# Kernel optimization log

Hardware: AMD Instinct MI355X
Metric: run time of the kernel (lower is better)

The kernel has to match this reference:

```python
import jax, jax.numpy as jnp
import numpy as np


def setup_inputs() -> dict:
    key = jax.random.key(0)
    k0, k1, k2, k3, k4, k5 = jax.random.split(key, 6)
    L1, L2, B, D = 512, 512, 32, 1024
    inputs1 = jax.random.normal(k0, (L1, B, D), dtype=jnp.float32)
    inputs2 = jax.random.normal(k1, (L2, B, D), dtype=jnp.float32)
    # mask value 0 marks a valid token (module keeps pairs where both masks == 0)
    mask1 = jax.random.randint(k2, (L1, B), 0, 2, dtype=jnp.int64)
    mask2 = jax.random.randint(k3, (L2, B), 0, 2, dtype=jnp.int64)
    W = jax.random.normal(k4, (D, D), dtype=jnp.float32) * 0.02
    b = jax.random.normal(k5, (1,), dtype=jnp.float32) * 0.02
    return {"inputs1": inputs1, "inputs2": inputs2, "mask1": mask1,
            "mask2": mask2, "W": W, "b": b, "k": 256}


def reference(inputs1, inputs2, mask1, mask2, W, b, k):
    # inputs: [len, bsz, hdim]; masks: [len, bsz]
    H1 = jnp.transpose(inputs1, (1, 0, 2))  # [B, L1, D]
    H2 = jnp.transpose(inputs2, (1, 0, 2))  # [B, L2, D]
    # bilinear scores: H1 @ W @ H2^T + b, then relu  -> [B, L1, L2]
    S = jax.nn.relu(jnp.einsum('bid,de,bje->bij', H1, W, H2) + b[0])
    # pair is valid iff both mask entries are 0
    valid = (mask1.T[:, :, None] == 0) & (mask2.T[:, None, :] == 0)  # [B, L1, L2]
    B = S.shape[0]
    S_flat = jnp.where(valid.reshape(B, -1), S.reshape(B, -1), -jnp.inf)
    num_elems = S_flat.shape[1]
    k_actual = min(k, num_elems)
    q, _ = jax.lax.top_k(S_flat, k_actual)  # [B, k_actual]
    # replace -inf tail entries with the last finite value in each row
    neg = jnp.isneginf(q)
    q_num_finite = k_actual - neg.sum(axis=-1)  # [B]
    fill = jnp.take_along_axis(q, (q_num_finite - 1)[:, None], axis=1)  # [B, 1]
    q = jnp.where(neg, fill, q)
    if k_actual < k:
        q = jnp.concatenate(
            [q, jnp.broadcast_to(q[:, -1:], (B, k - k_actual))], axis=1)
    return q
```

## Files before the change

kernel.cpp:

```cpp
#include <hip/hip_runtime.h>

typedef __bf16 bf16_t;
typedef bf16_t bf16x8 __attribute__((ext_vector_type(8)));
typedef float floatx4 __attribute__((ext_vector_type(4)));

#define L1C 512
#define L2C 512
#define BC  32
#define DC  1024
#define KTOP 256
#define NBIN 4096
#define CAP  1024
#define FBUF 16384

__device__ __forceinline__ unsigned short f2bf(float f) {
    unsigned u = __float_as_uint(f);
    u += 0x7FFFu + ((u >> 16) & 1u);
    return (unsigned short)(u >> 16);
}

__device__ __forceinline__ void g2l16(const unsigned short* g, unsigned short* l) {
    __builtin_amdgcn_global_load_lds((const unsigned int*)g, (unsigned int*)l,
                                     16, 0, 0);
}

__device__ __forceinline__ float decode_key(unsigned k) {
    return __uint_as_float(k & 0x7FFFFFFFu);
}

__global__ __launch_bounds__(256) void prep_kernel(
    const float* __restrict__ in1, const float* __restrict__ in2,
    const float* __restrict__ W,
    const int* __restrict__ mask1, const int* __restrict__ mask2,
    unsigned short* __restrict__ A1, unsigned short* __restrict__ A2,
    unsigned short* __restrict__ Wb,
    int* __restrict__ m1t, int* __restrict__ m2t,
    unsigned* __restrict__ cnt) {
    int r = blockIdx.x, t = threadIdx.x;
    if (r < 2 * L1C * BC + DC) {
        const float* src;
        unsigned short* dst;
        if (r < L1C * BC) {
            int l = r >> 5, b = r & 31;
            src = in1 + (size_t)r * DC;
            dst = A1 + ((size_t)b * L1C + l) * DC;
        } else if (r < 2 * L1C * BC) {
            int r2 = r - L1C * BC;
            int l = r2 >> 5, b = r2 & 31;
            src = in2 + (size_t)r2 * DC;
            dst = A2 + ((size_t)b * L2C + l) * DC;
        } else {
            int r3 = r - 2 * L1C * BC;
            src = W + (size_t)r3 * DC;
            dst = Wb + (size_t)r3 * DC;
        }
        float4 v = reinterpret_cast<const float4*>(src)[t];
        ushort4 o;
        o.x = f2bf(v.x); o.y = f2bf(v.y); o.z = f2bf(v.z); o.w = f2bf(v.w);
        reinterpret_cast<ushort4*>(dst)[t] = o;
    } else {
        int gid = (r - (2 * L1C * BC + DC)) * 256 + t;
        int l = gid & 511, b = gid >> 9;
        m1t[gid] = mask1[(l << 5) + b];
        m2t[gid] = mask2[(l << 5) + b];
        if (gid < BC * 16) cnt[gid] = 0;
    }
}

__global__ __launch_bounds__(256) void gemm1_kernel(
    const unsigned short* __restrict__ A,
    const unsigned short* __restrict__ Bt,
    unsigned short* __restrict__ C) {
    __shared__ unsigned short As[128][64];
    __shared__ unsigned short Bs[128][64];
    int tid = threadIdx.x;
    int wave = tid >> 6, lane = tid & 63;
    int lane15 = lane & 15, quad = lane >> 4;
    int wm = wave >> 1, wn = wave & 1;
    size_t m0 = (size_t)blockIdx.x * 128, n0 = (size_t)blockIdx.y * 128;

    floatx4 zero = {0.f, 0.f, 0.f, 0.f};
    floatx4 acc[4][4];
#pragma unroll
    for (int i = 0; i < 4; i++)
#pragma unroll
        for (int j = 0; j < 4; j++) acc[i][j] = zero;

    for (int k0 = 0; k0 < DC; k0 += 64) {
#pragma unroll
        for (int c = 0; c < 4; c++) {
            int cid = c * 256 + tid;
            int row = cid >> 3, col8 = (cid & 7) * 8;
            unsigned short* lbase = &As[0][0] + (c * 256 + wave * 64) * 8;
            g2l16(&A[(m0 + row) * DC + k0 + col8], lbase);
            unsigned short* lbase2 = &Bs[0][0] + (c * 256 + wave * 64) * 8;
            g2l16(&Bt[(n0 + row) * DC + k0 + col8], lbase2);
        }
        __syncthreads();
#pragma unroll
        for (int kk = 0; kk < 64; kk += 32) {
            bf16x8 af[4], bfr[4];
#pragma unroll
            for (int mi = 0; mi < 4; mi++)
                af[mi] = *reinterpret_cast<const bf16x8*>(
                    &As[wm * 64 + mi * 16 + lane15][kk + quad * 8]);
#pragma unroll
            for (int ni = 0; ni < 4; ni++)
                bfr[ni] = *reinterpret_cast<const bf16x8*>(
                    &Bs[wn * 64 + ni * 16 + lane15][kk + quad * 8]);
#pragma unroll
            for (int mi = 0; mi < 4; mi++)
#pragma unroll
                for (int ni = 0; ni < 4; ni++)
                    acc[mi][ni] = __builtin_amdgcn_mfma_f32_16x16x32_bf16(
                        af[mi], bfr[ni], acc[mi][ni], 0, 0, 0);
        }
        __syncthreads();
    }
#pragma unroll
    for (int mi = 0; mi < 4; mi++)
#pragma unroll
        for (int ni = 0; ni < 4; ni++)
#pragma unroll
            for (int r = 0; r < 4; r++) {
                size_t row = m0 + wm * 64 + mi * 16 + quad * 4 + r;
                size_t col = n0 + wn * 64 + ni * 16 + lane15;
                C[row * DC + col] = f2bf(acc[mi][ni][r]);
            }
}

__global__ __launch_bounds__(256) void gemm2_kernel(
    const unsigned short* __restrict__ A1,
    const unsigned short* __restrict__ V,
    const int* __restrict__ m1t, const int* __restrict__ m2t,
    const float* __restrict__ bptr,
    unsigned* __restrict__ cand,
    unsigned* __restrict__ cnt) {
    __shared__ unsigned short As[128][32];
    __shared__ unsigned short Bs[128][32];
    __shared__ unsigned lh[NBIN];
    __shared__ unsigned csum[256];
    __shared__ int m1s[128], m2s[128];
    __shared__ unsigned tsh, lcnt;
    int tid = threadIdx.x;
    int wave = tid >> 6, lane = tid & 63;
    int lane15 = lane & 15, quad = lane >> 4;
    int wm = wave >> 1, wn = wave & 1;
    int L = blockIdx.x;
    int xcd = L & 7, tile = (L >> 3) & 15, chunk = L >> 7;
    int b = xcd + (chunk << 3);
    int bx = tile & 3, by = tile >> 2;
    int m0 = bx * 128, n0 = by * 128;
    int gblk = b * 16 + by * 4 + bx;
    const unsigned short* Ab = A1 + (size_t)b * L1C * DC;
    const unsigned short* Bb = V + (size_t)b * L2C * DC;

    for (int i = tid; i < NBIN; i += 256) lh[i] = 0;
    if (tid < 128) m1s[tid] = (m1t[b * L1C + m0 + tid] == 0);
    else           m2s[tid - 128] = (m2t[b * L2C + n0 + tid - 128] == 0);

    floatx4 zero = {0.f, 0.f, 0.f, 0.f};
    floatx4 acc[4][4];
#pragma unroll
    for (int i = 0; i < 4; i++)
#pragma unroll
        for (int j = 0; j < 4; j++) acc[i][j] = zero;

    for (int k0 = 0; k0 < DC; k0 += 32) {
#pragma unroll
        for (int c = 0; c < 2; c++) {
            int cid = c * 256 + tid;
            int row = cid >> 2, col8 = (cid & 3) * 8;
            unsigned short* lbase = &As[0][0] + (c * 256 + wave * 64) * 8;
            g2l16(&Ab[(size_t)(m0 + row) * DC + k0 + col8], lbase);
            unsigned short* lbase2 = &Bs[0][0] + (c * 256 + wave * 64) * 8;
            g2l16(&Bb[(size_t)(n0 + row) * DC + k0 + col8], lbase2);
        }
        __syncthreads();
        bf16x8 af[4], bfr[4];
#pragma unroll
        for (int mi = 0; mi < 4; mi++)
            af[mi] = *reinterpret_cast<const bf16x8*>(&As[wm * 64 + mi * 16 + lane15][quad * 8]);
#pragma unroll
        for (int ni = 0; ni < 4; ni++)
            bfr[ni] = *reinterpret_cast<const bf16x8*>(&Bs[wn * 64 + ni * 16 + lane15][quad * 8]);
#pragma unroll
        for (int mi = 0; mi < 4; mi++)
#pragma unroll
            for (int ni = 0; ni < 4; ni++)
                acc[mi][ni] = __builtin_amdgcn_mfma_f32_16x16x32_bf16(
                    af[mi], bfr[ni], acc[mi][ni], 0, 0, 0);
        __syncthreads();
    }

    float bias = bptr[0];
    unsigned zc = 0;
#pragma unroll
    for (int ni = 0; ni < 4; ni++) {
        int jl = wn * 64 + ni * 16 + lane15;
        int v2 = m2s[jl];
#pragma unroll
        for (int mi = 0; mi < 4; mi++)
#pragma unroll
            for (int r = 0; r < 4; r++) {
                int il = wm * 64 + mi * 16 + quad * 4 + r;
                float s = acc[mi][ni][r] + bias;
                if (v2 && m1s[il]) {
                    if (s > 0.f)
                        atomicAdd(&lh[(__float_as_uint(s) | 0x80000000u) >> 20], 1u);
                    else
                        zc++;
                }
            }
    }
    if (zc) atomicAdd(&lh[2048], zc);
    __syncthreads();
    unsigned s16 = 0;
#pragma unroll
    for (int i = 0; i < 16; i++) s16 += lh[tid * 16 + i];
    csum[tid] = s16;
    __syncthreads();
    if (tid == 0) {
        unsigned cum = 0, bin = 2048;
        int found = 0;
        for (int c = 255; c >= 128 && !found; --c) {
            unsigned cs = csum[c];
            if (cum + cs >= KTOP) {
                for (int bb = c * 16 + 15; bb >= c * 16; --bb) {
                    unsigned h = lh[bb];
                    if (cum + h >= KTOP) { bin = (unsigned)bb; found = 1; break; }
                    cum += h;
                }
            } else cum += cs;
        }
        tsh = bin << 20;
        lcnt = 0;
    }
    __syncthreads();
    unsigned T = tsh;
    unsigned base = (unsigned)gblk * CAP;
#pragma unroll
    for (int ni = 0; ni < 4; ni++) {
        int jl = wn * 64 + ni * 16 + lane15;
        int v2 = m2s[jl];
#pragma unroll
        for (int mi = 0; mi < 4; mi++)
#pragma unroll
            for (int r = 0; r < 4; r++) {
                int il = wm * 64 + mi * 16 + quad * 4 + r;
                float s = acc[mi][ni][r] + bias;
                s = s > 0.f ? s : 0.f;
                unsigned key = (v2 && m1s[il])
                                   ? (__float_as_uint(s) | 0x80000000u) : 0u;
                if (key >= T) {
                    unsigned p = atomicAdd(&lcnt, 1u);
                    if (p < CAP) cand[base + p] = key;
                }
            }
    }
    __syncthreads();
    if (tid == 0) cnt[gblk] = lcnt < CAP ? lcnt : CAP;
}

__global__ __launch_bounds__(1024) void final_kernel(
    const unsigned* __restrict__ cand, const unsigned* __restrict__ cnt,
    float* __restrict__ out) {
    __shared__ unsigned buf[FBUF];
    __shared__ unsigned h[NBIN];
    __shared__ unsigned ss[256];
    __shared__ unsigned scnt_s[16], off_s[16];
    __shared__ unsigned ntot_s, sel_c, sel_a, B_s, R_s, mcount;
    __shared__ int have_s;
    __shared__ unsigned srt[256];
    int b = blockIdx.x, tid = threadIdx.x;
    int wv = tid >> 6, ln = tid & 63;

    if (tid < 16) {
        unsigned c = cnt[b * 16 + tid];
        scnt_s[tid] = c < CAP ? c : CAP;
    }
    __syncthreads();
    if (tid == 0) {
        unsigned o = 0;
        for (int i = 0; i < 16; i++) { off_s[i] = o; o += scnt_s[i]; }
        ntot_s = o;
        have_s = 1;
    }
    __syncthreads();
    {
        unsigned c = scnt_s[wv], o = off_s[wv];
        const unsigned* p = cand + (size_t)(b * 16 + wv) * CAP;
        for (unsigned i = ln; i < c; i += 64) buf[o + i] = p[i];
    }
    __syncthreads();
    unsigned n = ntot_s;

    unsigned Kr = KTOP;
    unsigned pfx = 0;
    unsigned kth = 0;
    for (int pass = 0; pass < 3; pass++) {
        int bins = (pass < 2) ? NBIN : 256;
        int shift = (pass == 0) ? 20 : (pass == 1) ? 8 : 0;
        int nch = bins >> 4;
        for (int i = tid; i < bins; i += 1024) h[i] = 0;
        __syncthreads();
        for (unsigned i = tid; i < n; i += 1024) {
            unsigned k = buf[i];
            bool ok = (pass == 0) ||
                      (pass == 1 && (k >> 20) == pfx) ||
                      (pass == 2 && (k >> 8) == pfx);
            if (ok) atomicAdd(&h[(k >> shift) & (bins - 1)], 1u);
        }
        __syncthreads();
        if (tid < nch) {
            unsigned s = 0;
#pragma unroll
            for (int i = 0; i < 16; i++) s += h[tid * 16 + i];
            ss[tid] = s;
        }
        __syncthreads();
        for (int off = 1; off < nch; off <<= 1) {
            unsigned v = 0;
            if (tid < nch && tid + (unsigned)off < (unsigned)nch) v = ss[tid + off];
            __syncthreads();
            if (tid < nch) ss[tid] += v;
            __syncthreads();
        }
        if (pass == 0) {
            if (tid == 0) have_s = (ss[0] >= KTOP);
            __syncthreads();
            if (!have_s) break;
        }
        if (tid < nch) {
            unsigned above = (tid + 1 < (unsigned)nch) ? ss[tid + 1] : 0u;
            if (above < Kr && ss[tid] >= Kr) { sel_c = tid; sel_a = above; }
        }
        __syncthreads();
        if (tid == 0) {
            unsigned cum = sel_a;
            for (int bb = (int)sel_c * 16 + 15; bb >= (int)sel_c * 16; --bb) {
                unsigned hb = h[bb];
                if (cum + hb >= Kr) { B_s = (unsigned)bb; R_s = Kr - cum; break; }
                cum += hb;
            }
        }
        __syncthreads();
        unsigned Bv = B_s;
        Kr = R_s;
        if (pass == 0) pfx = Bv;
        else if (pass == 1) pfx = (pfx << 12) | Bv;
        else kth = (pfx << 8) | Bv;
        __syncthreads();
    }

    if (tid == 0) mcount = 0;
    __syncthreads();
    int have = have_s;
    unsigned lim = have ? kth : 0u;
    for (unsigned i = tid; i < n; i += 1024) {
        unsigned k = buf[i];
        if (k > lim) {
            unsigned p = atomicAdd(&mcount, 1u);
            if (p < 256) srt[p] = k;
        }
    }
    __syncthreads();
    unsigned m = mcount;
    if (tid < 256 && tid >= (int)m) srt[tid] = have ? kth : 0u;
    for (int k2 = 2; k2 <= 256; k2 <<= 1) {
        for (int j2 = k2 >> 1; j2 > 0; j2 >>= 1) {
            __syncthreads();
            if (tid < 256) {
                int ixj = tid ^ j2;
                if (ixj > tid) {
                    unsigned a = srt[tid], c = srt[ixj];
                    bool up = (tid & k2) == 0;
                    if (up ? (a < c) : (a > c)) { srt[tid] = c; srt[ixj] = a; }
                }
            }
        }
    }
    __syncthreads();
    if (tid < 256) {
        unsigned nval = have ? KTOP : (m < KTOP ? m : KTOP);
        float v;
        if ((unsigned)tid < nval) v = decode_key(srt[tid]);
        else v = (nval > 0) ? decode_key(srt[nval - 1]) : -__builtin_inff();
        out[b * KTOP + tid] = v;
    }
}

extern "C" void kernel_launch(void* const* d_in, const int* in_sizes, int n_in,
                              void* d_out, int out_size, void* d_ws, size_t ws_size,
                              hipStream_t stream) {
    const float* in1   = (const float*)d_in[0];
    const float* in2   = (const float*)d_in[1];
    const int*   mask1 = (const int*)d_in[2];
    const int*   mask2 = (const int*)d_in[3];
    const float* W     = (const float*)d_in[4];
    const float* bias  = (const float*)d_in[5];
    float* out = (float*)d_out;

    char* ws = (char*)d_ws;
    size_t off = 0;
    const size_t nElem = (size_t)L1C * BC * DC;
    unsigned short* A1 = (unsigned short*)(ws + off); off += nElem * 2;
    unsigned short* A2 = (unsigned short*)(ws + off); off += nElem * 2;
    unsigned short* Wb = (unsigned short*)(ws + off); off += (size_t)DC * DC * 2;
    unsigned short* V  = (unsigned short*)(ws + off); off += nElem * 2;
    unsigned* cand = (unsigned*)(ws + off); off += (size_t)BC * 16 * CAP * 4;
    unsigned* cnt  = (unsigned*)(ws + off); off += (size_t)BC * 16 * 4;
    int* m1t = (int*)(ws + off); off += (size_t)BC * L1C * 4;
    int* m2t = (int*)(ws + off); off += (size_t)BC * L2C * 4;

    prep_kernel<<<2 * L1C * BC + DC + 64, 256, 0, stream>>>(
        in1, in2, W, mask1, mask2, A1, A2, Wb, m1t, m2t, cnt);
    gemm1_kernel<<<dim3(128, 8), 256, 0, stream>>>(A2, Wb, V);
    gemm2_kernel<<<512, 256, 0, stream>>>(A1, V, m1t, m2t, bias, cand, cnt);
    final_kernel<<<BC, 1024, 0, stream>>>(cand, cnt, out);
}
```

Before: 275.2 us.

## Compact valid tokens per batch before GEMMs and skip fully padded tiles

```diff
diff --git a/kernel.cpp b/kernel.cpp
--- a/kernel.cpp
+++ b/kernel.cpp
@@ -28,56 +28,85 @@
     return __uint_as_float(k & 0x7FFFFFFFu);
 }
 
+__global__ __launch_bounds__(512) void scan_kernel(
+    const int* __restrict__ mask1, const int* __restrict__ mask2,
+    int* __restrict__ idx1, int* __restrict__ idx2,
+    unsigned* __restrict__ nv1, unsigned* __restrict__ nv2,
+    unsigned* __restrict__ cnt) {
+    __shared__ unsigned sc[512];
+    int b = blockIdx.x, t = threadIdx.x;
+    for (int which = 0; which < 2; which++) {
+        const int* m = which ? mask2 : mask1;
+        int* idx = which ? idx2 : idx1;
+        unsigned v = (m[t * BC + b] == 0) ? 1u : 0u;
+        sc[t] = v;
+        __syncthreads();
+        for (int off = 1; off < 512; off <<= 1) {
+            unsigned x = (t >= off) ? sc[t - off] : 0u;
+            __syncthreads();
+            sc[t] += x;
+            __syncthreads();
+        }
+        if (v) idx[b * 512 + sc[t] - 1] = t;
+        if (t == 511) { if (which) nv2[b] = sc[511]; else nv1[b] = sc[511]; }
+        __syncthreads();
+    }
+    if (t < 16) cnt[b * 16 + t] = 0;
+}
+
 __global__ __launch_bounds__(256) void prep_kernel(
     const float* __restrict__ in1, const float* __restrict__ in2,
     const float* __restrict__ W,
-    const int* __restrict__ mask1, const int* __restrict__ mask2,
-    unsigned short* __restrict__ A1, unsigned short* __restrict__ A2,
-    unsigned short* __restrict__ Wb,
-    int* __restrict__ m1t, int* __restrict__ m2t,
-    unsigned* __restrict__ cnt) {
+    const int* __restrict__ idx1, const int* __restrict__ idx2,
+    const unsigned* __restrict__ nv1, const unsigned* __restrict__ nv2,
+    unsigned short* __restrict__ A1c, unsigned short* __restrict__ A2c,
+    unsigned short* __restrict__ Wb) {
     int r = blockIdx.x, t = threadIdx.x;
-    if (r < 2 * L1C * BC + DC) {
-        const float* src;
-        unsigned short* dst;
-        if (r < L1C * BC) {
-            int l = r >> 5, b = r & 31;
-            src = in1 + (size_t)r * DC;
-            dst = A1 + ((size_t)b * L1C + l) * DC;
-        } else if (r < 2 * L1C * BC) {
-            int r2 = r - L1C * BC;
-            int l = r2 >> 5, b = r2 & 31;
-            src = in2 + (size_t)r2 * DC;
-            dst = A2 + ((size_t)b * L2C + l) * DC;
+    const float* src;
+    unsigned short* dst;
+    if (r < 2 * 16384) {
+        int which = r >> 14;
+        int rr = r & 16383;
+        int b = rr >> 9, vi = rr & 511;
+        unsigned nv = which ? nv2[b] : nv1[b];
+        unsigned pad = (nv + 127u) & ~127u;
+        if ((unsigned)vi >= pad) return;
+        dst = (which ? A2c : A1c) + ((size_t)b * 512 + vi) * DC;
+        if ((unsigned)vi < nv) {
+            int l = (which ? idx2 : idx1)[b * 512 + vi];
+            src = (which ? in2 : in1) + (size_t)(l * BC + b) * DC;
         } else {
-            int r3 = r - 2 * L1C * BC;
-            src = W + (size_t)r3 * DC;
-            dst = Wb + (size_t)r3 * DC;
-        }
-        float4 v = reinterpret_cast<const float4*>(src)[t];
-        ushort4 o;
-        o.x = f2bf(v.x); o.y = f2bf(v.y); o.z = f2bf(v.z); o.w = f2bf(v.w);
-        reinterpret_cast<ushort4*>(dst)[t] = o;
+            ushort4 z = {0, 0, 0, 0};
+            reinterpret_cast<ushort4*>(dst)[t] = z;
+            return;
+        }
     } else {
-        int gid = (r - (2 * L1C * BC + DC)) * 256 + t;
-        int l = gid & 511, b = gid >> 9;
-        m1t[gid] = mask1[(l << 5) + b];
-        m2t[gid] = mask2[(l << 5) + b];
-        if (gid < BC * 16) cnt[gid] = 0;
-    }
+        int r3 = r - 2 * 16384;
+        src = W + (size_t)r3 * DC;
+        dst = Wb + (size_t)r3 * DC;
+    }
+    float4 v = reinterpret_cast<const float4*>(src)[t];
+    ushort4 o;
+    o.x = f2bf(v.x); o.y = f2bf(v.y); o.z = f2bf(v.z); o.w = f2bf(v.w);
+    reinterpret_cast<ushort4*>(dst)[t] = o;
 }
 
 __global__ __launch_bounds__(256) void gemm1_kernel(
     const unsigned short* __restrict__ A,
     const unsigned short* __restrict__ Bt,
-    unsigned short* __restrict__ C) {
-    __shared__ unsigned short As[128][64];
-    __shared__ unsigned short Bs[128][64];
+    unsigned short* __restrict__ C,
+    const unsigned* __restrict__ nv2) {
+    int bi = blockIdx.x >> 2, mt = blockIdx.x & 3;
+    unsigned pad2 = (nv2[bi] + 127u) & ~127u;
+    if ((unsigned)(mt * 128) >= pad2) return;
+    __shared__ unsigned short As[128][32];
+    __shared__ unsigned short Bs[128][32];
     int tid = threadIdx.x;
     int wave = tid >> 6, lane = tid & 63;
     int lane15 = lane & 15, quad = lane >> 4;
     int wm = wave >> 1, wn = wave & 1;
-    size_t m0 = (size_t)blockIdx.x * 128, n0 = (size_t)blockIdx.y * 128;
+    size_t m0 = (size_t)bi * 512 + mt * 128;
+    size_t n0 = (size_t)blockIdx.y * 128;
 
     floatx4 zero = {0.f, 0.f, 0.f, 0.f};
     floatx4 acc[4][4];
@@ -86,35 +115,30 @@
 #pragma unroll
         for (int j = 0; j < 4; j++) acc[i][j] = zero;
 
-    for (int k0 = 0; k0 < DC; k0 += 64) {
-#pragma unroll
-        for (int c = 0; c < 4; c++) {
+    for (int k0 = 0; k0 < DC; k0 += 32) {
+#pragma unroll
+        for (int c = 0; c < 2; c++) {
             int cid = c * 256 + tid;
-            int row = cid >> 3, col8 = (cid & 7) * 8;
+            int row = cid >> 2, col8 = (cid & 3) * 8;
             unsigned short* lbase = &As[0][0] + (c * 256 + wave * 64) * 8;
             g2l16(&A[(m0 + row) * DC + k0 + col8], lbase);
             unsigned short* lbase2 = &Bs[0][0] + (c * 256 + wave * 64) * 8;
             g2l16(&Bt[(n0 + row) * DC + k0 + col8], lbase2);
         }
         __syncthreads();
-#pragma unroll
-        for (int kk = 0; kk < 64; kk += 32) {
-            bf16x8 af[4], bfr[4];
-#pragma unroll
-            for (int mi = 0; mi < 4; mi++)
-                af[mi] = *reinterpret_cast<const bf16x8*>(
-                    &As[wm * 64 + mi * 16 + lane15][kk + quad * 8]);
+        bf16x8 af[4], bfr[4];
+#pragma unroll
+        for (int mi = 0; mi < 4; mi++)
+            af[mi] = *reinterpret_cast<const bf16x8*>(&As[wm * 64 + mi * 16 + lane15][quad * 8]);
+#pragma unroll
+        for (int ni = 0; ni < 4; ni++)
+            bfr[ni] = *reinterpret_cast<const bf16x8*>(&Bs[wn * 64 + ni * 16 + lane15][quad * 8]);
+#pragma unroll
+        for (int mi = 0; mi < 4; mi++)
 #pragma unroll
             for (int ni = 0; ni < 4; ni++)
-                bfr[ni] = *reinterpret_cast<const bf16x8*>(
-                    &Bs[wn * 64 + ni * 16 + lane15][kk + quad * 8]);
-#pragma unroll
-            for (int mi = 0; mi < 4; mi++)
-#pragma unroll
-                for (int ni = 0; ni < 4; ni++)
-                    acc[mi][ni] = __builtin_amdgcn_mfma_f32_16x16x32_bf16(
-                        af[mi], bfr[ni], acc[mi][ni], 0, 0, 0);
-        }
+                acc[mi][ni] = __builtin_amdgcn_mfma_f32_16x16x32_bf16(
+                    af[mi], bfr[ni], acc[mi][ni], 0, 0, 0);
         __syncthreads();
     }
 #pragma unroll
@@ -130,34 +154,37 @@
 }
 
 __global__ __launch_bounds__(256) void gemm2_kernel(
-    const unsigned short* __restrict__ A1,
+    const unsigned short* __restrict__ A1c,
     const unsigned short* __restrict__ V,
-    const int* __restrict__ m1t, const int* __restrict__ m2t,
+    const unsigned* __restrict__ nv1, const unsigned* __restrict__ nv2,
     const float* __restrict__ bptr,
     unsigned* __restrict__ cand,
     unsigned* __restrict__ cnt) {
-    __shared__ unsigned short As[128][32];
-    __shared__ unsigned short Bs[128][32];
-    __shared__ unsigned lh[NBIN];
-    __shared__ unsigned csum[256];
-    __shared__ int m1s[128], m2s[128];
-    __shared__ unsigned tsh, lcnt;
-    int tid = threadIdx.x;
-    int wave = tid >> 6, lane = tid & 63;
-    int lane15 = lane & 15, quad = lane >> 4;
-    int wm = wave >> 1, wn = wave & 1;
     int L = blockIdx.x;
     int xcd = L & 7, tile = (L >> 3) & 15, chunk = L >> 7;
     int b = xcd + (chunk << 3);
     int bx = tile & 3, by = tile >> 2;
     int m0 = bx * 128, n0 = by * 128;
     int gblk = b * 16 + by * 4 + bx;
-    const unsigned short* Ab = A1 + (size_t)b * L1C * DC;
-    const unsigned short* Bb = V + (size_t)b * L2C * DC;
+    int tid = threadIdx.x;
+    unsigned nv1v = nv1[b], nv2v = nv2[b];
+    unsigned pad1 = (nv1v + 127u) & ~127u, pad2 = (nv2v + 127u) & ~127u;
+    if ((unsigned)m0 >= pad1 || (unsigned)n0 >= pad2) {
+        if (tid == 0) cnt[gblk] = 0;
+        return;
+    }
+    __shared__ unsigned short As[128][32];
+    __shared__ unsigned short Bs[128][32];
+    __shared__ unsigned lh[NBIN];
+    __shared__ unsigned csum[256];
+    __shared__ unsigned tsh, lcnt, zeq;
+    int wave = tid >> 6, lane = tid & 63;
+    int lane15 = lane & 15, quad = lane >> 4;
+    int wm = wave >> 1, wn = wave & 1;
+    const unsigned short* Ab = A1c + (size_t)b * 512 * DC;
+    const unsigned short* Bb = V + (size_t)b * 512 * DC;
 
     for (int i = tid; i < NBIN; i += 256) lh[i] = 0;
-    if (tid < 128) m1s[tid] = (m1t[b * L1C + m0 + tid] == 0);
-    else           m2s[tid - 128] = (m2t[b * L2C + n0 + tid - 128] == 0);
 
     floatx4 zero = {0.f, 0.f, 0.f, 0.f};
     floatx4 acc[4][4];
@@ -197,15 +224,15 @@
     unsigned zc = 0;
 #pragma unroll
     for (int ni = 0; ni < 4; ni++) {
-        int jl = wn * 64 + ni * 16 + lane15;
-        int v2 = m2s[jl];
+        int jl = n0 + wn * 64 + ni * 16 + lane15;
+        int v2 = (unsigned)jl < nv2v;
 #pragma unroll
         for (int mi = 0; mi < 4; mi++)
 #pragma unroll
             for (int r = 0; r < 4; r++) {
-                int il = wm * 64 + mi * 16 + quad * 4 + r;
+                int il = m0 + wm * 64 + mi * 16 + quad * 4 + r;
                 float s = acc[mi][ni][r] + bias;
-                if (v2 && m1s[il]) {
+                if (v2 && (unsigned)il < nv1v) {
                     if (s > 0.f)
                         atomicAdd(&lh[(__float_as_uint(s) | 0x80000000u) >> 20], 1u);
                     else
@@ -235,26 +262,33 @@
         }
         tsh = bin << 20;
         lcnt = 0;
+        zeq = 0;
     }
     __syncthreads();
     unsigned T = tsh;
     unsigned base = (unsigned)gblk * CAP;
 #pragma unroll
     for (int ni = 0; ni < 4; ni++) {
-        int jl = wn * 64 + ni * 16 + lane15;
-        int v2 = m2s[jl];
+        int jl = n0 + wn * 64 + ni * 16 + lane15;
+        int v2 = (unsigned)jl < nv2v;
 #pragma unroll
         for (int mi = 0; mi < 4; mi++)
 #pragma unroll
             for (int r = 0; r < 4; r++) {
-                int il = wm * 64 + mi * 16 + quad * 4 + r;
+                int il = m0 + wm * 64 + mi * 16 + quad * 4 + r;
                 float s = acc[mi][ni][r] + bias;
                 s = s > 0.f ? s : 0.f;
-                unsigned key = (v2 && m1s[il])
+                unsigned key = (v2 && (unsigned)il < nv1v)
                                    ? (__float_as_uint(s) | 0x80000000u) : 0u;
-                if (key >= T) {
+                if (key > T) {
                     unsigned p = atomicAdd(&lcnt, 1u);
                     if (p < CAP) cand[base + p] = key;
+                } else if (key == T) {
+                    unsigned z = atomicAdd(&zeq, 1u);
+                    if (z < KTOP) {
+                        unsigned p = atomicAdd(&lcnt, 1u);
+                        if (p < CAP) cand[base + p] = key;
+                    }
                 }
             }
     }
@@ -403,19 +437,22 @@
 
     char* ws = (char*)d_ws;
     size_t off = 0;
-    const size_t nElem = (size_t)L1C * BC * DC;
-    unsigned short* A1 = (unsigned short*)(ws + off); off += nElem * 2;
-    unsigned short* A2 = (unsigned short*)(ws + off); off += nElem * 2;
-    unsigned short* Wb = (unsigned short*)(ws + off); off += (size_t)DC * DC * 2;
-    unsigned short* V  = (unsigned short*)(ws + off); off += nElem * 2;
+    const size_t nElem = (size_t)512 * BC * DC;
+    unsigned short* A1c = (unsigned short*)(ws + off); off += nElem * 2;
+    unsigned short* A2c = (unsigned short*)(ws + off); off += nElem * 2;
+    unsigned short* Wb  = (unsigned short*)(ws + off); off += (size_t)DC * DC * 2;
+    unsigned short* V   = (unsigned short*)(ws + off); off += nElem * 2;
     unsigned* cand = (unsigned*)(ws + off); off += (size_t)BC * 16 * CAP * 4;
     unsigned* cnt  = (unsigned*)(ws + off); off += (size_t)BC * 16 * 4;
-    int* m1t = (int*)(ws + off); off += (size_t)BC * L1C * 4;
-    int* m2t = (int*)(ws + off); off += (size_t)BC * L2C * 4;
-
-    prep_kernel<<<2 * L1C * BC + DC + 64, 256, 0, stream>>>(
-        in1, in2, W, mask1, mask2, A1, A2, Wb, m1t, m2t, cnt);
-    gemm1_kernel<<<dim3(128, 8), 256, 0, stream>>>(A2, Wb, V);
-    gemm2_kernel<<<512, 256, 0, stream>>>(A1, V, m1t, m2t, bias, cand, cnt);
+    int* idx1 = (int*)(ws + off); off += (size_t)BC * 512 * 4;
+    int* idx2 = (int*)(ws + off); off += (size_t)BC * 512 * 4;
+    unsigned* nv1 = (unsigned*)(ws + off); off += BC * 4;
+    unsigned* nv2 = (unsigned*)(ws + off); off += BC * 4;
+
+    scan_kernel<<<BC, 512, 0, stream>>>(mask1, mask2, idx1, idx2, nv1, nv2, cnt);
+    prep_kernel<<<2 * 16384 + 1024, 256, 0, stream>>>(
+        in1, in2, W, idx1, idx2, nv1, nv2, A1c, A2c, Wb);
+    gemm1_kernel<<<dim3(128, 8), 256, 0, stream>>>(A2c, Wb, V, nv2);
+    gemm2_kernel<<<512, 256, 0, stream>>>(A1c, V, nv1, nv2, bias, cand, cnt);
     final_kernel<<<BC, 1024, 0, stream>>>(cand, cnt, out);
 }
```

Result: faster. 263.2 us (-4.4%).
